# Performance work log

Measured on AMD Instinct MI355X. Metric: run time of the kernel, lower is better.

The kernel has to match this reference:

```python
import jax, jax.numpy as jnp
import numpy as np

N = 100000        # nodes
E = 1600000       # edges (avg degree 16)
D_NODE = 32
D_EDGE = 16
H = 64
C = 5


def setup_inputs() -> dict:
    key = jax.random.key(0)
    ks = jax.random.split(key, 11)
    x = jax.random.normal(ks[0], (N, D_NODE), jnp.float32)
    edge_index = jax.random.randint(ks[1], (2, E), 0, N, jnp.int32)
    edge_attr = jax.random.normal(ks[2], (E, D_EDGE), jnp.float32)
    W1 = jax.random.normal(ks[3], (D_NODE, H), jnp.float32) / np.sqrt(D_NODE)
    b1 = jax.random.normal(ks[4], (H,), jnp.float32) * 0.02
    W2 = jax.random.normal(ks[5], (H, H), jnp.float32) / np.sqrt(H)
    b2 = jax.random.normal(ks[6], (H,), jnp.float32) * 0.02
    Wc1 = jax.random.normal(ks[7], (2 * H + D_EDGE, 64), jnp.float32) / np.sqrt(2 * H + D_EDGE)
    bc1 = jax.random.normal(ks[8], (64,), jnp.float32) * 0.02
    Wc2 = jax.random.normal(ks[9], (64, C), jnp.float32) / np.sqrt(64)
    bc2 = jax.random.normal(ks[10], (C,), jnp.float32) * 0.02
    return {"x": x, "edge_index": edge_index, "edge_attr": edge_attr,
            "W1": W1, "b1": b1, "W2": W2, "b2": b2,
            "Wc1": Wc1, "bc1": bc1, "Wc2": Wc2, "bc2": bc2}


def gcn_conv(x, W, b, src, dst, n):
    h = x @ W                                   # [n, H]
    loop = jnp.arange(n, dtype=src.dtype)
    s = jnp.concatenate([src, loop])            # self-loops appended
    d = jnp.concatenate([dst, loop])
    deg = jax.ops.segment_sum(jnp.ones_like(s, h.dtype), d, num_segments=n)
    dinv = jax.lax.rsqrt(deg)                   # deg >= 1 due to self-loops
    norm = dinv[s] * dinv[d]                    # [E+n]
    out = jax.ops.segment_sum(h[s] * norm[:, None], d, num_segments=n)
    return out + b


def reference(x, edge_index, edge_attr, W1, b1, W2, b2, Wc1, bc1, Wc2, bc2):
    src, dst = edge_index[0], edge_index[1]
    n = x.shape[0]
    h = jax.nn.relu(gcn_conv(x, W1, b1, src, dst, n))
    h = gcn_conv(h, W2, b2, src, dst, n)
    # gather-concat edge features: [E, 2H + D_EDGE]
    ef = jnp.concatenate([h[src], h[dst], edge_attr], axis=1)
    out = jax.nn.relu(ef @ Wc1 + bc1) @ Wc2 + bc2
    return out
```

## Files before the change

kernel.cpp:

```cpp
#include <hip/hip_runtime.h>
#include <hip/hip_bf16.h>


typedef __attribute__((ext_vector_type(8))) short  bf16x8;
typedef __attribute__((ext_vector_type(16))) float f32x16;

__device__ inline short f2bf(float f)
{
    union { float f; unsigned u; } v; v.f = f;
    unsigned r = v.u + 0x7fff + ((v.u >> 16) & 1);
    return (short)(r >> 16);
}

__device__ inline float2 bfp2f(unsigned u)
{
    union { unsigned u; float f; } a, b;
    a.u = u << 16;
    b.u = u & 0xffff0000u;
    return make_float2(a.f, b.f);
}

__device__ inline unsigned packbf2(float a, float b)
{
    return (unsigned)(unsigned short)f2bf(a) | ((unsigned)(unsigned short)f2bf(b) << 16);
}


__global__ __launch_bounds__(256) void k_bcount(const int* __restrict__ ei, int* __restrict__ bcnt, int E)
{
    __shared__ int h[512];
    for (int i = threadIdx.x; i < 512; i += 256) h[i] = 0;
    __syncthreads();
    for (long e = (long)blockIdx.x * 256 + threadIdx.x; e < E; e += (long)gridDim.x * 256)
        atomicAdd(&h[ei[E + e] >> 8], 1);
    __syncthreads();
    for (int i = threadIdx.x; i < 512; i += 256)
        if (h[i]) atomicAdd(&bcnt[i], h[i]);
}

__global__ __launch_bounds__(512) void k_bscan(const int* __restrict__ bcnt, int nbk, int* __restrict__ bstart)
{
    __shared__ int s[512];
    int t = threadIdx.x;
    int v = (t < nbk) ? bcnt[t] : 0;
    s[t] = v;
    __syncthreads();
    for (int o = 1; o < 512; o <<= 1) {
        int a = (t >= o) ? s[t - o] : 0;
        __syncthreads();
        s[t] += a;
        __syncthreads();
    }
    if (t < nbk) bstart[t + 1] = s[t];
    if (t == 0) bstart[0] = 0;
}

__global__ __launch_bounds__(256) void k_binscatter(const int* __restrict__ ei, const int* __restrict__ bstart,
                                                    int* __restrict__ bcur, int2* __restrict__ ebs, int E)
{
    __shared__ int cnt[512], gb[512];
    const int tid = threadIdx.x;
    for (int i = tid; i < 512; i += 256) cnt[i] = 0;
    __syncthreads();
    const int base = blockIdx.x * 4096;
    int d[16], lp[16];
#pragma unroll
    for (int i = 0; i < 16; ++i) {
        int e = base + i * 256 + tid;
        if (e < E) {
            d[i] = ei[E + e];
            lp[i] = atomicAdd(&cnt[d[i] >> 8], 1);
        } else d[i] = -1;
    }
    __syncthreads();
    for (int i = tid; i < 512; i += 256) gb[i] = cnt[i] ? atomicAdd(&bcur[i], cnt[i]) : 0;
    __syncthreads();
#pragma unroll
    for (int i = 0; i < 16; ++i) {
        if (d[i] >= 0) {
            int e = base + i * 256 + tid;
            int b = d[i] >> 8;
            int2 p;
            p.x = ei[e];
            p.y = d[i];
            ebs[(size_t)bstart[b] + gb[b] + lp[i]] = p;
        }
    }
}

__global__ __launch_bounds__(256) void k_build(const int2* __restrict__ ebs, const int* __restrict__ bstart,
                                               int* __restrict__ rs, int* __restrict__ col,
                                               float* __restrict__ dinv, int N, int E)
{
    __shared__ int cnt[256], lstart[256], cnt2[256];
    const int b = blockIdx.x;
    const int base = b << 8;
    const int tid = threadIdx.x;
    cnt[tid] = 0; cnt2[tid] = 0;
    __syncthreads();
    const int s0 = bstart[b], s1 = bstart[b + 1];
    for (int i = s0 + tid; i < s1; i += 256) atomicAdd(&cnt[ebs[i].y - base], 1);
    __syncthreads();
    const int v = cnt[tid];
    lstart[tid] = v;
    __syncthreads();
    for (int o = 1; o < 256; o <<= 1) {
        int a = (tid >= o) ? lstart[tid - o] : 0;
        __syncthreads();
        lstart[tid] += a;
        __syncthreads();
    }
    const int node = base + tid;
    if (node < N) {
        rs[node] = s0 + lstart[tid] - v;
        dinv[node] = rsqrtf((float)(v + 1));
    }
    if (b == 0 && tid == 0) rs[N] = E;
    __syncthreads();
    for (int i = s0 + tid; i < s1; i += 256) {
        int2 p = ebs[i];
        int ln = p.y - base;
        int pos = atomicAdd(&cnt2[ln], 1);
        col[s0 + (lstart[ln] - cnt[ln]) + pos] = p.x;
    }
}

__global__ __launch_bounds__(256) void k_prep(const float* __restrict__ Wc1, const float* __restrict__ Wc2,
                                              const float* __restrict__ W2, const float* __restrict__ W1,
                                              short* __restrict__ Wc1T, short* __restrict__ Wc2T,
                                              short* __restrict__ W2T, short* __restrict__ W1T)
{
    int t = blockIdx.x * 256 + threadIdx.x;
    if (t < 9216) {
        int j = t / 144, k = t - j * 144;
        Wc1T[t] = f2bf(Wc1[k * 64 + j]);
    } else if (t < 11264) {
        int u = t - 9216;
        int rr = u / 64, k = u - rr * 64;
        Wc2T[u] = (rr < 5) ? f2bf(Wc2[k * 5 + rr]) : (short)0;
    } else if (t < 15360) {
        int u = t - 11264;
        int j = u / 64, k = u - j * 64;
        W2T[u] = f2bf(W2[k * 64 + j]);
    } else if (t < 17408) {
        int u = t - 15360;
        int j = u / 32, k = u - j * 32;
        W1T[u] = f2bf(W1[k * 64 + j]);
    }
}

__global__ __launch_bounds__(256) void k_xs(const float* __restrict__ x, const float* __restrict__ dinv,
                                            unsigned short* __restrict__ xs, int n)
{
    int id = blockIdx.x * 256 + threadIdx.x;
    int v = id >> 4, l = id & 15;
    if (v >= n) return;
    float2 xv = *(const float2*)&x[(size_t)v * 32 + l * 2];
    float dv = dinv[v];
    *(unsigned*)(xs + (size_t)v * 32 + l * 2) = packbf2(xv.x * dv, xv.y * dv);
}

__global__ __launch_bounds__(256) void k_ea(const float* __restrict__ ea, unsigned short* __restrict__ eabf, long n4)
{
    long id = (long)blockIdx.x * 256 + threadIdx.x;
    if (id >= n4) return;
    float4 v = *(const float4*)&ea[id * 4];
    short4 o;
    o.x = f2bf(v.x); o.y = f2bf(v.y); o.z = f2bf(v.z); o.w = f2bf(v.w);
    *(short4*)&eabf[id * 4] = o;
}

__global__ __launch_bounds__(256) void k_agg_x(const unsigned short* __restrict__ xs,
                                               const float* __restrict__ dinv,
                                               const int* __restrict__ rs, const int* __restrict__ col,
                                               unsigned short* __restrict__ xagg, int n)
{
    const int tid = threadIdx.x;
    const int l   = tid & 15;
    const int v   = blockIdx.x * 16 + (tid >> 4);
    if (v >= n) return;

    float2 acc = bfp2f(*(const unsigned*)(xs + (size_t)v * 32 + l * 2));
    int i = rs[v];
    const int end = rs[v + 1];
    for (; i + 8 <= end; i += 8) {
        int c0 = col[i],     c1 = col[i + 1], c2 = col[i + 2], c3 = col[i + 3];
        int c4 = col[i + 4], c5 = col[i + 5], c6 = col[i + 6], c7 = col[i + 7];
        unsigned u0 = *(const unsigned*)(xs + (size_t)c0 * 32 + l * 2);
        unsigned u1 = *(const unsigned*)(xs + (size_t)c1 * 32 + l * 2);
        unsigned u2 = *(const unsigned*)(xs + (size_t)c2 * 32 + l * 2);
        unsigned u3 = *(const unsigned*)(xs + (size_t)c3 * 32 + l * 2);
        unsigned u4 = *(const unsigned*)(xs + (size_t)c4 * 32 + l * 2);
        unsigned u5 = *(const unsigned*)(xs + (size_t)c5 * 32 + l * 2);
        unsigned u6 = *(const unsigned*)(xs + (size_t)c6 * 32 + l * 2);
        unsigned u7 = *(const unsigned*)(xs + (size_t)c7 * 32 + l * 2);
        float2 a0 = bfp2f(u0), a1 = bfp2f(u1), a2 = bfp2f(u2), a3 = bfp2f(u3);
        float2 a4 = bfp2f(u4), a5 = bfp2f(u5), a6 = bfp2f(u6), a7 = bfp2f(u7);
        acc.x += (a0.x + a1.x) + (a2.x + a3.x) + (a4.x + a5.x) + (a6.x + a7.x);
        acc.y += (a0.y + a1.y) + (a2.y + a3.y) + (a4.y + a5.y) + (a6.y + a7.y);
    }
    for (; i < end; ++i) {
        float2 a = bfp2f(*(const unsigned*)(xs + (size_t)col[i] * 32 + l * 2));
        acc.x += a.x; acc.y += a.y;
    }
    const float dv = dinv[v];
    *(unsigned*)(xagg + (size_t)v * 32 + l * 2) = packbf2(dv * acc.x, dv * acc.y);
}

__global__ __launch_bounds__(256) void k_agg64(const unsigned short* __restrict__ hsc,
                                               const float* __restrict__ dinv,
                                               const int* __restrict__ rs, const int* __restrict__ col,
                                               unsigned short* __restrict__ out, int n)
{
    const int tid = threadIdx.x;
    const int l   = tid & 31;
    const int v   = blockIdx.x * 8 + (tid >> 5);
    if (v >= n) return;

    float2 acc = bfp2f(*(const unsigned*)(hsc + (size_t)v * 64 + l * 2));
    int i = rs[v];
    const int end = rs[v + 1];
    for (; i + 8 <= end; i += 8) {
        int c0 = col[i],     c1 = col[i + 1], c2 = col[i + 2], c3 = col[i + 3];
        int c4 = col[i + 4], c5 = col[i + 5], c6 = col[i + 6], c7 = col[i + 7];
        unsigned u0 = *(const unsigned*)(hsc + (size_t)c0 * 64 + l * 2);
        unsigned u1 = *(const unsigned*)(hsc + (size_t)c1 * 64 + l * 2);
        unsigned u2 = *(const unsigned*)(hsc + (size_t)c2 * 64 + l * 2);
        unsigned u3 = *(const unsigned*)(hsc + (size_t)c3 * 64 + l * 2);
        unsigned u4 = *(const unsigned*)(hsc + (size_t)c4 * 64 + l * 2);
        unsigned u5 = *(const unsigned*)(hsc + (size_t)c5 * 64 + l * 2);
        unsigned u6 = *(const unsigned*)(hsc + (size_t)c6 * 64 + l * 2);
        unsigned u7 = *(const unsigned*)(hsc + (size_t)c7 * 64 + l * 2);
        float2 a0 = bfp2f(u0), a1 = bfp2f(u1), a2 = bfp2f(u2), a3 = bfp2f(u3);
        float2 a4 = bfp2f(u4), a5 = bfp2f(u5), a6 = bfp2f(u6), a7 = bfp2f(u7);
        acc.x += (a0.x + a1.x) + (a2.x + a3.x) + (a4.x + a5.x) + (a6.x + a7.x);
        acc.y += (a0.y + a1.y) + (a2.y + a3.y) + (a4.y + a5.y) + (a6.y + a7.y);
    }
    for (; i < end; ++i) {
        float2 a = bfp2f(*(const unsigned*)(hsc + (size_t)col[i] * 64 + l * 2));
        acc.x += a.x; acc.y += a.y;
    }
    const float dv = dinv[v];
    *(unsigned*)(out + (size_t)v * 64 + l * 2) = packbf2(dv * acc.x, dv * acc.y);
}

__global__ __launch_bounds__(256) void k_node1(const unsigned short* __restrict__ xagg,
                                               const short* __restrict__ W1T,
                                               const float* __restrict__ b1, const float* __restrict__ dinv,
                                               unsigned short* __restrict__ h1s, int n)
{
    const int tid = threadIdx.x;
    const int w = tid >> 6, lane = tid & 63, r = lane & 31, kg = lane >> 5;
    const int nb = blockIdx.x * 128 + w * 32;

    bf16x8 a0[2], a1[2];
#pragma unroll
    for (int t = 0; t < 2; ++t) {
        a0[t] = *(const bf16x8*)&W1T[r * 32 + t * 16 + kg * 8];
        a1[t] = *(const bf16x8*)&W1T[(r + 32) * 32 + t * 16 + kg * 8];
    }

    int row = nb + r;
    if (row >= n) row = n - 1;
    f32x16 acc0 = {0.f}, acc1 = {0.f};
#pragma unroll
    for (int t = 0; t < 2; ++t) {
        bf16x8 b = *(const bf16x8*)&xagg[(size_t)row * 32 + t * 16 + kg * 8];
        acc0 = __builtin_amdgcn_mfma_f32_32x32x16_bf16(a0[t], b, acc0, 0, 0, 0);
        acc1 = __builtin_amdgcn_mfma_f32_32x32x16_bf16(a1[t], b, acc1, 0, 0, 0);
    }

    const int node = nb + r;
    if (node < n) {
        const float dv = dinv[node];
#pragma unroll
        for (int q = 0; q < 4; ++q) {
            const int j0 = 8 * q + 4 * kg;
            float4 bA = *(const float4*)&b1[j0];
            float4 bB = *(const float4*)&b1[j0 + 32];
            short4 s0, s1;
            float t0, t1;
            t0 = acc0[4 * q]     + bA.x; t0 = t0 > 0.f ? t0 : 0.f; s0.x = f2bf(t0 * dv);
            t0 = acc0[4 * q + 1] + bA.y; t0 = t0 > 0.f ? t0 : 0.f; s0.y = f2bf(t0 * dv);
            t0 = acc0[4 * q + 2] + bA.z; t0 = t0 > 0.f ? t0 : 0.f; s0.z = f2bf(t0 * dv);
            t0 = acc0[4 * q + 3] + bA.w; t0 = t0 > 0.f ? t0 : 0.f; s0.w = f2bf(t0 * dv);
            t1 = acc1[4 * q]     + bB.x; t1 = t1 > 0.f ? t1 : 0.f; s1.x = f2bf(t1 * dv);
            t1 = acc1[4 * q + 1] + bB.y; t1 = t1 > 0.f ? t1 : 0.f; s1.y = f2bf(t1 * dv);
            t1 = acc1[4 * q + 2] + bB.z; t1 = t1 > 0.f ? t1 : 0.f; s1.z = f2bf(t1 * dv);
            t1 = acc1[4 * q + 3] + bB.w; t1 = t1 > 0.f ? t1 : 0.f; s1.w = f2bf(t1 * dv);
            *(short4*)&h1s[(size_t)node * 64 + j0]      = s0;
            *(short4*)&h1s[(size_t)node * 64 + j0 + 32] = s1;
        }
    }
}

__global__ __launch_bounds__(256) void k_node2(const unsigned short* __restrict__ xagg2,
                                               const short* __restrict__ W2T,
                                               const float* __restrict__ b2,
                                               unsigned short* __restrict__ h2, int n)
{
    const int tid = threadIdx.x;
    const int w = tid >> 6, lane = tid & 63, r = lane & 31, kg = lane >> 5;
    const int nb = blockIdx.x * 128 + w * 32;

    bf16x8 a0[4], a1[4];
#pragma unroll
    for (int t = 0; t < 4; ++t) {
        a0[t] = *(const bf16x8*)&W2T[r * 64 + t * 16 + kg * 8];
        a1[t] = *(const bf16x8*)&W2T[(r + 32) * 64 + t * 16 + kg * 8];
    }

    int row = nb + r;
    if (row >= n) row = n - 1;
    f32x16 acc0 = {0.f}, acc1 = {0.f};
#pragma unroll
    for (int t = 0; t < 4; ++t) {
        bf16x8 b = *(const bf16x8*)&xagg2[(size_t)row * 64 + t * 16 + kg * 8];
        acc0 = __builtin_amdgcn_mfma_f32_32x32x16_bf16(a0[t], b, acc0, 0, 0, 0);
        acc1 = __builtin_amdgcn_mfma_f32_32x32x16_bf16(a1[t], b, acc1, 0, 0, 0);
    }

    const int node = nb + r;
    if (node < n) {
#pragma unroll
        for (int q = 0; q < 4; ++q) {
            const int j0 = 8 * q + 4 * kg;
            float4 bA = *(const float4*)&b2[j0];
            float4 bB = *(const float4*)&b2[j0 + 32];
            short4 s0, s1;
            s0.x = f2bf(acc0[4 * q]     + bA.x); s0.y = f2bf(acc0[4 * q + 1] + bA.y);
            s0.z = f2bf(acc0[4 * q + 2] + bA.z); s0.w = f2bf(acc0[4 * q + 3] + bA.w);
            s1.x = f2bf(acc1[4 * q]     + bB.x); s1.y = f2bf(acc1[4 * q + 1] + bB.y);
            s1.z = f2bf(acc1[4 * q + 2] + bB.z); s1.w = f2bf(acc1[4 * q + 3] + bB.w);
            *(short4*)&h2[(size_t)node * 64 + j0]      = s0;
            *(short4*)&h2[(size_t)node * 64 + j0 + 32] = s1;
        }
    }
}

template <int ABF>
__global__ __launch_bounds__(256) void k_edge_mlp_mfma(
    const unsigned short* __restrict__ h2bf, const void* __restrict__ eattr,
    const int* __restrict__ ei,
    const short* __restrict__ Wc1T, const float* __restrict__ bc1,
    const short* __restrict__ Wc2T, const float* __restrict__ bc2,
    float* __restrict__ out, int E)
{
    __shared__ char slab[4 * 8192];

    const int tid = threadIdx.x;
    const int w = tid >> 6, lane = tid & 63, r = lane & 31, kg = lane >> 5;
    const int q = lane & 3, sr = lane >> 2;

    char* myslab = slab + w * 8192;
    short* hid = (short*)myslab;

    const long eb = (long)blockIdx.x * 128 + w * 32;
    long ecl = eb + r; if (ecl >= E) ecl = E - 1;
    const int ns = ei[ecl];
    const int nd = ei[E + ecl];

    bf16x8 aa;
    if (ABF) {
        aa = *(const bf16x8*)((const unsigned short*)eattr + (size_t)ecl * 16 + kg * 8);
    } else {
        const float* arow = (const float*)eattr + (size_t)ecl * 16;
        float4 alo = *(const float4*)&arow[kg * 8];
        float4 ahi = *(const float4*)&arow[kg * 8 + 4];
        aa[0] = f2bf(alo.x); aa[1] = f2bf(alo.y); aa[2] = f2bf(alo.z); aa[3] = f2bf(alo.w);
        aa[4] = f2bf(ahi.x); aa[5] = f2bf(ahi.y); aa[6] = f2bf(ahi.z); aa[7] = f2bf(ahi.w);
    }

    {
        int n0 = __shfl(ns, sr);
        int n1 = __shfl(ns, 16 + sr);
        int m0 = __shfl(nd, sr);
        int m1 = __shfl(nd, 16 + sr);
        int4 s0 = *(const int4*)&h2bf[(size_t)n0 * 64 + q * 8];
        int4 s1 = *(const int4*)&h2bf[(size_t)n0 * 64 + 32 + q * 8];
        int4 s2 = *(const int4*)&h2bf[(size_t)n1 * 64 + q * 8];
        int4 s3 = *(const int4*)&h2bf[(size_t)n1 * 64 + 32 + q * 8];
        int4 d0 = *(const int4*)&h2bf[(size_t)m0 * 64 + q * 8];
        int4 d1 = *(const int4*)&h2bf[(size_t)m0 * 64 + 32 + q * 8];
        int4 d2 = *(const int4*)&h2bf[(size_t)m1 * 64 + q * 8];
        int4 d3 = *(const int4*)&h2bf[(size_t)m1 * 64 + 32 + q * 8];
        const int x0 = (sr ^ q) * 16, x1 = (16 + (sr ^ q)) * 16;
        *(int4*)(myslab + q * 512 + x0)              = s0;
        *(int4*)(myslab + (4 + q) * 512 + x0)        = s1;
        *(int4*)(myslab + q * 512 + x1)              = s2;
        *(int4*)(myslab + (4 + q) * 512 + x1)        = s3;
        *(int4*)(myslab + 4096 + q * 512 + x0)       = d0;
        *(int4*)(myslab + 4096 + (4 + q) * 512 + x0) = d1;
        *(int4*)(myslab + 4096 + q * 512 + x1)       = d2;
        *(int4*)(myslab + 4096 + (4 + q) * 512 + x1) = d3;
    }

    f32x16 acc0, acc1;
    const float bias0 = bc1[r], bias1 = bc1[r + 32];
#pragma unroll
    for (int i = 0; i < 16; ++i) { acc0[i] = bias0; acc1[i] = bias1; }

#pragma unroll
    for (int t = 0; t < 4; ++t) {
        const int c = 2 * t + kg;
        bf16x8 a  = *(const bf16x8*)(myslab + c * 512 + ((r ^ (c & 3)) * 16));
        bf16x8 w0 = *(const bf16x8*)&Wc1T[r * 144 + t * 16 + kg * 8];
        bf16x8 w1 = *(const bf16x8*)&Wc1T[(r + 32) * 144 + t * 16 + kg * 8];
        acc0 = __builtin_amdgcn_mfma_f32_32x32x16_bf16(a, w0, acc0, 0, 0, 0);
        acc1 = __builtin_amdgcn_mfma_f32_32x32x16_bf16(a, w1, acc1, 0, 0, 0);
    }
#pragma unroll
    for (int t = 0; t < 4; ++t) {
        const int c = 2 * t + kg;
        bf16x8 a  = *(const bf16x8*)(myslab + 4096 + c * 512 + ((r ^ (c & 3)) * 16));
        bf16x8 w0 = *(const bf16x8*)&Wc1T[r * 144 + (4 + t) * 16 + kg * 8];
        bf16x8 w1 = *(const bf16x8*)&Wc1T[(r + 32) * 144 + (4 + t) * 16 + kg * 8];
        acc0 = __builtin_amdgcn_mfma_f32_32x32x16_bf16(a, w0, acc0, 0, 0, 0);
        acc1 = __builtin_amdgcn_mfma_f32_32x32x16_bf16(a, w1, acc1, 0, 0, 0);
    }
    {
        bf16x8 w0 = *(const bf16x8*)&Wc1T[r * 144 + 128 + kg * 8];
        bf16x8 w1 = *(const bf16x8*)&Wc1T[(r + 32) * 144 + 128 + kg * 8];
        acc0 = __builtin_amdgcn_mfma_f32_32x32x16_bf16(aa, w0, acc0, 0, 0, 0);
        acc1 = __builtin_amdgcn_mfma_f32_32x32x16_bf16(aa, w1, acc1, 0, 0, 0);
    }

#pragma unroll
    for (int reg = 0; reg < 16; ++reg) {
        const int row = (reg & 3) + 8 * (reg >> 2) + 4 * kg;
        const int sw  = (row & 7) << 4;
        float v0 = acc0[reg]; v0 = v0 > 0.f ? v0 : 0.f;
        float v1 = acc1[reg]; v1 = v1 > 0.f ? v1 : 0.f;
        hid[row * 64 + ((((r)      << 1) ^ sw) >> 1)] = f2bf(v0);
        hid[row * 64 + ((((r + 32) << 1) ^ sw) >> 1)] = f2bf(v1);
    }

    const int sw2 = (r & 7) << 4;
    const float bias2 = (r < 5) ? bc2[r] : 0.f;
    f32x16 acc2;
#pragma unroll
    for (int i = 0; i < 16; ++i) acc2[i] = bias2;
#pragma unroll
    for (int t2 = 0; t2 < 4; ++t2) {
        const int boff = (t2 * 32 + kg * 16) ^ sw2;
        bf16x8 a  = *(const bf16x8*)((const char*)&hid[r * 64] + boff);
        bf16x8 bw = *(const bf16x8*)&Wc2T[r * 64 + t2 * 16 + kg * 8];
        acc2 = __builtin_amdgcn_mfma_f32_32x32x16_bf16(a, bw, acc2, 0, 0, 0);
    }

#pragma unroll
    for (int reg = 0; reg < 16; ++reg) {
        const int row = (reg & 3) + 8 * (reg >> 2) + 4 * kg;
        const long eo = eb + row;
        if (r < 5 && eo < E) out[(size_t)eo * 5 + r] = acc2[reg];
    }
}

extern "C" void kernel_launch(void* const* d_in, const int* in_sizes, int n_in,
                              void* d_out, int out_size, void* d_ws, size_t ws_size,
                              hipStream_t stream)
{
    const float* x     = (const float*)d_in[0];
    const int*   ei    = (const int*)d_in[1];
    const float* eattr = (const float*)d_in[2];
    const float* W1    = (const float*)d_in[3];
    const float* b1    = (const float*)d_in[4];
    const float* W2    = (const float*)d_in[5];
    const float* b2    = (const float*)d_in[6];
    const float* Wc1   = (const float*)d_in[7];
    const float* bc1   = (const float*)d_in[8];
    const float* Wc2   = (const float*)d_in[9];
    const float* bc2   = (const float*)d_in[10];
    float* outp = (float*)d_out;

    const int N = in_sizes[0] / 32;
    const int E = in_sizes[1] / 2;
    const int nbk = (N + 255) >> 8;

    size_t off = 0;
    char* base = (char*)d_ws;
    auto carve = [&](size_t bytes) -> void* {
        void* p = base + off;
        off += (bytes + 255) & ~(size_t)255;
        return p;
    };
    int*   bcnt   = (int*)carve(1024 * 4);
    int*   bcur   = bcnt + 512;
    int*   bstart = (int*)carve(520 * 4);
    float* dinv   = (float*)carve((size_t)N * 4);
    int*   rs     = (int*)carve((size_t)(N + 1) * 4);
    int*   col    = (int*)carve((size_t)E * 4);
    int2*  ebs    = (int2*)carve((size_t)E * 8);
    unsigned short* xs    = (unsigned short*)carve((size_t)N * 32 * 2);
    unsigned short* xagg  = (unsigned short*)carve((size_t)N * 32 * 2);
    unsigned short* h1s   = (unsigned short*)carve((size_t)N * 64 * 2);
    unsigned short* xagg2 = (unsigned short*)carve((size_t)N * 64 * 2);
    unsigned short* h2bf  = h1s;
    short* Wc1T   = (short*)carve(9216 * 2);
    short* Wc2T   = (short*)carve(2048 * 2);
    short* W2T    = (short*)carve(4096 * 2);
    short* W1T    = (short*)carve(2048 * 2);
    unsigned short* eabf = (unsigned short*)carve((size_t)E * 16 * 2);
    const bool use_abf = (off <= ws_size);
    (void)n_in; (void)out_size;

    const int NAX = (N + 15) / 16;
    const int NA = (N + 7) / 8;
    const int NM = (N + 127) / 128;
    const int NT = (E + 127) / 128;
    const int NSC = (E + 4095) / 4096;

    hipMemsetAsync(bcnt, 0, 1024 * 4, stream);

    k_prep<<<68, 256, 0, stream>>>(Wc1, Wc2, W2, W1, Wc1T, Wc2T, W2T, W1T);
    if (use_abf) k_ea<<<(int)(((long)E * 4 + 255) / 256), 256, 0, stream>>>(eattr, eabf, (long)E * 4);

    k_bcount<<<1024, 256, 0, stream>>>(ei, bcnt, E);
    k_bscan<<<1, 512, 0, stream>>>(bcnt, nbk, bstart);
    k_binscatter<<<NSC, 256, 0, stream>>>(ei, bstart, bcur, ebs, E);
    k_build<<<nbk, 256, 0, stream>>>(ebs, bstart, rs, col, dinv, N, E);

    k_xs<<<(N * 16 + 255) / 256, 256, 0, stream>>>(x, dinv, xs, N);
    k_agg_x<<<NAX, 256, 0, stream>>>(xs, dinv, rs, col, xagg, N);
    k_node1<<<NM, 256, 0, stream>>>(xagg, W1T, b1, dinv, h1s, N);
    k_agg64<<<NA, 256, 0, stream>>>(h1s, dinv, rs, col, xagg2, N);
    k_node2<<<NM, 256, 0, stream>>>(xagg2, W2T, b2, h2bf, N);

    if (use_abf)
        k_edge_mlp_mfma<1><<<NT, 256, 0, stream>>>(h2bf, eabf, ei, Wc1T, bc1, Wc2T, bc2, outp, E);
    else
        k_edge_mlp_mfma<0><<<NT, 256, 0, stream>>>(h2bf, eattr, ei, Wc1T, bc1, Wc2T, bc2, outp, E);
}
```

Before: 314.7 us.

## Fuse xs scaling into CSR build, drop edge-attr bf16 pass, widen gathers

Folds the dinv-scaled bf16 conversion of x into the CSR build kernel, removing the separate k_xs launch. Drops the pre-pass that converted edge_attr to bf16, so the edge MLP now reads fp32 attributes directly and converts them in registers. The aggregation kernels now load 8 bytes per lane with half as many lanes per node. The hidden-layer store in the edge MLP packs two bf16 values per 32-bit write, which requires permuting the Wc2T row order to match. Together these remove launches and roughly 100 MB of extra attribute traffic, at the cost of more work per thread and a reordered weight layout.

```diff
diff --git a/kernel.cpp b/kernel.cpp
--- a/kernel.cpp
+++ b/kernel.cpp
@@ -24,7 +24,6 @@
 {
     return (unsigned)(unsigned short)f2bf(a) | ((unsigned)(unsigned short)f2bf(b) << 16);
 }
-
 
 __global__ __launch_bounds__(256) void k_bcount(const int* __restrict__ ei, int* __restrict__ bcnt, int E)
 {
@@ -90,7 +89,9 @@
 
 __global__ __launch_bounds__(256) void k_build(const int2* __restrict__ ebs, const int* __restrict__ bstart,
                                                int* __restrict__ rs, int* __restrict__ col,
-                                               float* __restrict__ dinv, int N, int E)
+                                               float* __restrict__ dinv,
+                                               const float* __restrict__ x, unsigned short* __restrict__ xs,
+                                               int N, int E)
 {
     __shared__ int cnt[256], lstart[256], cnt2[256];
     const int b = blockIdx.x;
@@ -122,6 +123,17 @@
         int ln = p.y - base;
         int pos = atomicAdd(&cnt2[ln], 1);
         col[s0 + (lstart[ln] - cnt[ln]) + pos] = p.x;
+    }
+#pragma unroll
+    for (int i = 0; i < 16; ++i) {
+        int id = i * 256 + tid;
+        int ni = id >> 4, pr = id & 15;
+        int nd = base + ni;
+        if (nd < N) {
+            float dv = rsqrtf((float)(cnt[ni] + 1));
+            float2 xv = *(const float2*)&x[(size_t)nd * 32 + pr * 2];
+            *(unsigned*)(xs + (size_t)nd * 32 + pr * 2) = packbf2(xv.x * dv, xv.y * dv);
+        }
     }
 }
 
@@ -136,7 +148,8 @@
         Wc1T[t] = f2bf(Wc1[k * 64 + j]);
     } else if (t < 11264) {
         int u = t - 9216;
-        int rr = u / 64, k = u - rr * 64;
+        int rr = u / 64, p = u - rr * 64;
+        int k = (p >> 1) + ((p & 1) << 5);
         Wc2T[u] = (rr < 5) ? f2bf(Wc2[k * 5 + rr]) : (short)0;
     } else if (t < 15360) {
         int u = t - 11264;
@@ -149,62 +162,52 @@
     }
 }
 
-__global__ __launch_bounds__(256) void k_xs(const float* __restrict__ x, const float* __restrict__ dinv,
-                                            unsigned short* __restrict__ xs, int n)
-{
-    int id = blockIdx.x * 256 + threadIdx.x;
-    int v = id >> 4, l = id & 15;
-    if (v >= n) return;
-    float2 xv = *(const float2*)&x[(size_t)v * 32 + l * 2];
-    float dv = dinv[v];
-    *(unsigned*)(xs + (size_t)v * 32 + l * 2) = packbf2(xv.x * dv, xv.y * dv);
-}
-
-__global__ __launch_bounds__(256) void k_ea(const float* __restrict__ ea, unsigned short* __restrict__ eabf, long n4)
-{
-    long id = (long)blockIdx.x * 256 + threadIdx.x;
-    if (id >= n4) return;
-    float4 v = *(const float4*)&ea[id * 4];
-    short4 o;
-    o.x = f2bf(v.x); o.y = f2bf(v.y); o.z = f2bf(v.z); o.w = f2bf(v.w);
-    *(short4*)&eabf[id * 4] = o;
-}
-
 __global__ __launch_bounds__(256) void k_agg_x(const unsigned short* __restrict__ xs,
                                                const float* __restrict__ dinv,
                                                const int* __restrict__ rs, const int* __restrict__ col,
                                                unsigned short* __restrict__ xagg, int n)
 {
     const int tid = threadIdx.x;
-    const int l   = tid & 15;
-    const int v   = blockIdx.x * 16 + (tid >> 4);
+    const int l   = tid & 7;
+    const int v   = blockIdx.x * 32 + (tid >> 3);
     if (v >= n) return;
 
-    float2 acc = bfp2f(*(const unsigned*)(xs + (size_t)v * 32 + l * 2));
+    uint2 sv = *(const uint2*)(xs + (size_t)v * 32 + l * 4);
+    float2 aL = bfp2f(sv.x), aH = bfp2f(sv.y);
     int i = rs[v];
     const int end = rs[v + 1];
     for (; i + 8 <= end; i += 8) {
         int c0 = col[i],     c1 = col[i + 1], c2 = col[i + 2], c3 = col[i + 3];
         int c4 = col[i + 4], c5 = col[i + 5], c6 = col[i + 6], c7 = col[i + 7];
-        unsigned u0 = *(const unsigned*)(xs + (size_t)c0 * 32 + l * 2);
-        unsigned u1 = *(const unsigned*)(xs + (size_t)c1 * 32 + l * 2);
-        unsigned u2 = *(const unsigned*)(xs + (size_t)c2 * 32 + l * 2);
-        unsigned u3 = *(const unsigned*)(xs + (size_t)c3 * 32 + l * 2);
-        unsigned u4 = *(const unsigned*)(xs + (size_t)c4 * 32 + l * 2);
-        unsigned u5 = *(const unsigned*)(xs + (size_t)c5 * 32 + l * 2);
-        unsigned u6 = *(const unsigned*)(xs + (size_t)c6 * 32 + l * 2);
-        unsigned u7 = *(const unsigned*)(xs + (size_t)c7 * 32 + l * 2);
-        float2 a0 = bfp2f(u0), a1 = bfp2f(u1), a2 = bfp2f(u2), a3 = bfp2f(u3);
-        float2 a4 = bfp2f(u4), a5 = bfp2f(u5), a6 = bfp2f(u6), a7 = bfp2f(u7);
-        acc.x += (a0.x + a1.x) + (a2.x + a3.x) + (a4.x + a5.x) + (a6.x + a7.x);
-        acc.y += (a0.y + a1.y) + (a2.y + a3.y) + (a4.y + a5.y) + (a6.y + a7.y);
+        uint2 u0 = *(const uint2*)(xs + (size_t)c0 * 32 + l * 4);
+        uint2 u1 = *(const uint2*)(xs + (size_t)c1 * 32 + l * 4);
+        uint2 u2 = *(const uint2*)(xs + (size_t)c2 * 32 + l * 4);
+        uint2 u3 = *(const uint2*)(xs + (size_t)c3 * 32 + l * 4);
+        uint2 u4 = *(const uint2*)(xs + (size_t)c4 * 32 + l * 4);
+        uint2 u5 = *(const uint2*)(xs + (size_t)c5 * 32 + l * 4);
+        uint2 u6 = *(const uint2*)(xs + (size_t)c6 * 32 + l * 4);
+        uint2 u7 = *(const uint2*)(xs + (size_t)c7 * 32 + l * 4);
+        float2 p;
+        p = bfp2f(u0.x); aL.x += p.x; aL.y += p.y; p = bfp2f(u0.y); aH.x += p.x; aH.y += p.y;
+        p = bfp2f(u1.x); aL.x += p.x; aL.y += p.y; p = bfp2f(u1.y); aH.x += p.x; aH.y += p.y;
+        p = bfp2f(u2.x); aL.x += p.x; aL.y += p.y; p = bfp2f(u2.y); aH.x += p.x; aH.y += p.y;
+        p = bfp2f(u3.x); aL.x += p.x; aL.y += p.y; p = bfp2f(u3.y); aH.x += p.x; aH.y += p.y;
+        p = bfp2f(u4.x); aL.x += p.x; aL.y += p.y; p = bfp2f(u4.y); aH.x += p.x; aH.y += p.y;
+        p = bfp2f(u5.x); aL.x += p.x; aL.y += p.y; p = bfp2f(u5.y); aH.x += p.x; aH.y += p.y;
+        p = bfp2f(u6.x); aL.x += p.x; aL.y += p.y; p = bfp2f(u6.y); aH.x += p.x; aH.y += p.y;
+        p = bfp2f(u7.x); aL.x += p.x; aL.y += p.y; p = bfp2f(u7.y); aH.x += p.x; aH.y += p.y;
     }
     for (; i < end; ++i) {
-        float2 a = bfp2f(*(const unsigned*)(xs + (size_t)col[i] * 32 + l * 2));
-        acc.x += a.x; acc.y += a.y;
+        uint2 u = *(const uint2*)(xs + (size_t)col[i] * 32 + l * 4);
+        float2 p;
+        p = bfp2f(u.x); aL.x += p.x; aL.y += p.y;
+        p = bfp2f(u.y); aH.x += p.x; aH.y += p.y;
     }
     const float dv = dinv[v];
-    *(unsigned*)(xagg + (size_t)v * 32 + l * 2) = packbf2(dv * acc.x, dv * acc.y);
+    uint2 o;
+    o.x = packbf2(dv * aL.x, dv * aL.y);
+    o.y = packbf2(dv * aH.x, dv * aH.y);
+    *(uint2*)(xagg + (size_t)v * 32 + l * 4) = o;
 }
 
 __global__ __launch_bounds__(256) void k_agg64(const unsigned short* __restrict__ hsc,
@@ -213,35 +216,46 @@
                                                unsigned short* __restrict__ out, int n)
 {
     const int tid = threadIdx.x;
-    const int l   = tid & 31;
-    const int v   = blockIdx.x * 8 + (tid >> 5);
+    const int l   = tid & 15;
+    const int v   = blockIdx.x * 16 + (tid >> 4);
     if (v >= n) return;
 
-    float2 acc = bfp2f(*(const unsigned*)(hsc + (size_t)v * 64 + l * 2));
+    uint2 sv = *(const uint2*)(hsc + (size_t)v * 64 + l * 4);
+    float2 aL = bfp2f(sv.x), aH = bfp2f(sv.y);
     int i = rs[v];
     const int end = rs[v + 1];
     for (; i + 8 <= end; i += 8) {
         int c0 = col[i],     c1 = col[i + 1], c2 = col[i + 2], c3 = col[i + 3];
         int c4 = col[i + 4], c5 = col[i + 5], c6 = col[i + 6], c7 = col[i + 7];
-        unsigned u0 = *(const unsigned*)(hsc + (size_t)c0 * 64 + l * 2);
-        unsigned u1 = *(const unsigned*)(hsc + (size_t)c1 * 64 + l * 2);
-        unsigned u2 = *(const unsigned*)(hsc + (size_t)c2 * 64 + l * 2);
-        unsigned u3 = *(const unsigned*)(hsc + (size_t)c3 * 64 + l * 2);
-        unsigned u4 = *(const unsigned*)(hsc + (size_t)c4 * 64 + l * 2);
-        unsigned u5 = *(const unsigned*)(hsc + (size_t)c5 * 64 + l * 2);
-        unsigned u6 = *(const unsigned*)(hsc + (size_t)c6 * 64 + l * 2);
-        unsigned u7 = *(const unsigned*)(hsc + (size_t)c7 * 64 + l * 2);
-        float2 a0 = bfp2f(u0), a1 = bfp2f(u1), a2 = bfp2f(u2), a3 = bfp2f(u3);
-        float2 a4 = bfp2f(u4), a5 = bfp2f(u5), a6 = bfp2f(u6), a7 = bfp2f(u7);
-        acc.x += (a0.x + a1.x) + (a2.x + a3.x) + (a4.x + a5.x) + (a6.x + a7.x);
-        acc.y += (a0.y + a1.y) + (a2.y + a3.y) + (a4.y + a5.y) + (a6.y + a7.y);
+        uint2 u0 = *(const uint2*)(hsc + (size_t)c0 * 64 + l * 4);
+        uint2 u1 = *(const uint2*)(hsc + (size_t)c1 * 64 + l * 4);
+        uint2 u2 = *(const uint2*)(hsc + (size_t)c2 * 64 + l * 4);
+        uint2 u3 = *(const uint2*)(hsc + (size_t)c3 * 64 + l * 4);
+        uint2 u4 = *(const uint2*)(hsc + (size_t)c4 * 64 + l * 4);
+        uint2 u5 = *(const uint2*)(hsc + (size_t)c5 * 64 + l * 4);
+        uint2 u6 = *(const uint2*)(hsc + (size_t)c6 * 64 + l * 4);
+        uint2 u7 = *(const uint2*)(hsc + (size_t)c7 * 64 + l * 4);
+        float2 p;
+        p = bfp2f(u0.x); aL.x += p.x; aL.y += p.y; p = bfp2f(u0.y); aH.x += p.x; aH.y += p.y;
+        p = bfp2f(u1.x); aL.x += p.x; aL.y += p.y; p = bfp2f(u1.y); aH.x += p.x; aH.y += p.y;
+        p = bfp2f(u2.x); aL.x += p.x; aL.y += p.y; p = bfp2f(u2.y); aH.x += p.x; aH.y += p.y;
+        p = bfp2f(u3.x); aL.x += p.x; aL.y += p.y; p = bfp2f(u3.y); aH.x += p.x; aH.y += p.y;
+        p = bfp2f(u4.x); aL.x += p.x; aL.y += p.y; p = bfp2f(u4.y); aH.x += p.x; aH.y += p.y;
+        p = bfp2f(u5.x); aL.x += p.x; aL.y += p.y; p = bfp2f(u5.y); aH.x += p.x; aH.y += p.y;
+        p = bfp2f(u6.x); aL.x += p.x; aL.y += p.y; p = bfp2f(u6.y); aH.x += p.x; aH.y += p.y;
+        p = bfp2f(u7.x); aL.x += p.x; aL.y += p.y; p = bfp2f(u7.y); aH.x += p.x; aH.y += p.y;
     }
     for (; i < end; ++i) {
-        float2 a = bfp2f(*(const unsigned*)(hsc + (size_t)col[i] * 64 + l * 2));
-        acc.x += a.x; acc.y += a.y;
+        uint2 u = *(const uint2*)(hsc + (size_t)col[i] * 64 + l * 4);
+        float2 p;
+        p = bfp2f(u.x); aL.x += p.x; aL.y += p.y;
+        p = bfp2f(u.y); aH.x += p.x; aH.y += p.y;
     }
     const float dv = dinv[v];
-    *(unsigned*)(out + (size_t)v * 64 + l * 2) = packbf2(dv * acc.x, dv * acc.y);
+    uint2 o;
+    o.x = packbf2(dv * aL.x, dv * aL.y);
+    o.y = packbf2(dv * aH.x, dv * aH.y);
+    *(uint2*)(out + (size_t)v * 64 + l * 4) = o;
 }
 
 __global__ __launch_bounds__(256) void k_node1(const unsigned short* __restrict__ xagg,
@@ -338,9 +352,8 @@
     }
 }
 
-template <int ABF>
 __global__ __launch_bounds__(256) void k_edge_mlp_mfma(
-    const unsigned short* __restrict__ h2bf, const void* __restrict__ eattr,
+    const unsigned short* __restrict__ h2bf, const float* __restrict__ eattr,
     const int* __restrict__ ei,
     const short* __restrict__ Wc1T, const float* __restrict__ bc1,
     const short* __restrict__ Wc2T, const float* __restrict__ bc2,
@@ -353,7 +366,6 @@
     const int q = lane & 3, sr = lane >> 2;
 
     char* myslab = slab + w * 8192;
-    short* hid = (short*)myslab;
 
     const long eb = (long)blockIdx.x * 128 + w * 32;
     long ecl = eb + r; if (ecl >= E) ecl = E - 1;
@@ -361,10 +373,8 @@
     const int nd = ei[E + ecl];
 
     bf16x8 aa;
-    if (ABF) {
-        aa = *(const bf16x8*)((const unsigned short*)eattr + (size_t)ecl * 16 + kg * 8);
-    } else {
-        const float* arow = (const float*)eattr + (size_t)ecl * 16;
+    {
+        const float* arow = &eattr[(size_t)ecl * 16];
         float4 alo = *(const float4*)&arow[kg * 8];
         float4 ahi = *(const float4*)&arow[kg * 8 + 4];
         aa[0] = f2bf(alo.x); aa[1] = f2bf(alo.y); aa[2] = f2bf(alo.z); aa[3] = f2bf(alo.w);
@@ -428,22 +438,19 @@
 #pragma unroll
     for (int reg = 0; reg < 16; ++reg) {
         const int row = (reg & 3) + 8 * (reg >> 2) + 4 * kg;
-        const int sw  = (row & 7) << 4;
         float v0 = acc0[reg]; v0 = v0 > 0.f ? v0 : 0.f;
         float v1 = acc1[reg]; v1 = v1 > 0.f ? v1 : 0.f;
-        hid[row * 64 + ((((r)      << 1) ^ sw) >> 1)] = f2bf(v0);
-        hid[row * 64 + ((((r + 32) << 1) ^ sw) >> 1)] = f2bf(v1);
-    }
-
-    const int sw2 = (r & 7) << 4;
+        *(unsigned*)(myslab + row * 128 + ((4 * r) ^ ((row & 7) << 4))) = packbf2(v0, v1);
+    }
+
     const float bias2 = (r < 5) ? bc2[r] : 0.f;
     f32x16 acc2;
 #pragma unroll
     for (int i = 0; i < 16; ++i) acc2[i] = bias2;
 #pragma unroll
     for (int t2 = 0; t2 < 4; ++t2) {
-        const int boff = (t2 * 32 + kg * 16) ^ sw2;
-        bf16x8 a  = *(const bf16x8*)((const char*)&hid[r * 64] + boff);
+        const int m = t2 * 2 + kg;
+        bf16x8 a  = *(const bf16x8*)(myslab + r * 128 + ((16 * m) ^ ((r & 7) << 4)));
         bf16x8 bw = *(const bf16x8*)&Wc2T[r * 64 + t2 * 16 + kg * 8];
         acc2 = __builtin_amdgcn_mfma_f32_32x32x16_bf16(a, bw, acc2, 0, 0, 0);
     }
@@ -500,34 +507,27 @@
     short* Wc2T   = (short*)carve(2048 * 2);
     short* W2T    = (short*)carve(4096 * 2);
     short* W1T    = (short*)carve(2048 * 2);
-    unsigned short* eabf = (unsigned short*)carve((size_t)E * 16 * 2);
-    const bool use_abf = (off <= ws_size);
-    (void)n_in; (void)out_size;
-
-    const int NAX = (N + 15) / 16;
-    const int NA = (N + 7) / 8;
-    const int NM = (N + 127) / 128;
-    const int NT = (E + 127) / 128;
+    (void)n_in; (void)out_size; (void)ws_size;
+
+    const int NAX = (N + 31) / 32;
+    const int NA  = (N + 15) / 16;
+    const int NM  = (N + 127) / 128;
+    const int NT  = (E + 127) / 128;
     const int NSC = (E + 4095) / 4096;
 
     hipMemsetAsync(bcnt, 0, 1024 * 4, stream);
 
     k_prep<<<68, 256, 0, stream>>>(Wc1, Wc2, W2, W1, Wc1T, Wc2T, W2T, W1T);
-    if (use_abf) k_ea<<<(int)(((long)E * 4 + 255) / 256), 256, 0, stream>>>(eattr, eabf, (long)E * 4);
 
     k_bcount<<<1024, 256, 0, stream>>>(ei, bcnt, E);
     k_bscan<<<1, 512, 0, stream>>>(bcnt, nbk, bstart);
     k_binscatter<<<NSC, 256, 0, stream>>>(ei, bstart, bcur, ebs, E);
-    k_build<<<nbk, 256, 0, stream>>>(ebs, bstart, rs, col, dinv, N, E);
-
-    k_xs<<<(N * 16 + 255) / 256, 256, 0, stream>>>(x, dinv, xs, N);
+    k_build<<<nbk, 256, 0, stream>>>(ebs, bstart, rs, col, dinv, x, xs, N, E);
+
     k_agg_x<<<NAX, 256, 0, stream>>>(xs, dinv, rs, col, xagg, N);
     k_node1<<<NM, 256, 0, stream>>>(xagg, W1T, b1, dinv, h1s, N);
     k_agg64<<<NA, 256, 0, stream>>>(h1s, dinv, rs, col, xagg2, N);
     k_node2<<<NM, 256, 0, stream>>>(xagg2, W2T, b2, h2bf, N);
 
-    if (use_abf)
-        k_edge_mlp_mfma<1><<<NT, 256, 0, stream>>>(h2bf, eabf, ei, Wc1T, bc1, Wc2T, bc2, outp, E);
-    else
-        k_edge_mlp_mfma<0><<<NT, 256, 0, stream>>>(h2bf, eattr, ei, Wc1T, bc1, Wc2T, bc2, outp, E);
-}
+    k_edge_mlp_mfma<<<NT, 256, 0, stream>>>(h2bf, eattr, ei, Wc1T, bc1, Wc2T, bc2, outp, E);
+}
```

Measured after the change: 287.5 us. 1.09x faster.
